# Optimization experiments

Measured on AMD Instinct MI355X. Metric: run time of the kernel, lower is better.

The kernel has to match this reference:

```python
import jax, jax.numpy as jnp
import numpy as np

LOG_0 = -1.0e30          # finite stand-in for log(0); avoids -inf NaNs under vjp
ACTIVE = -1.0e29         # anything above this is an 'active' beam
PRUNE_LOGIT = -9.0       # original skips extensions with log-prob <= -9


def _decode_one(probs, length, beam_width, blank_index):
    """CTC prefix beam search for one example. probs: [T, V] log-probs."""
    T, V = probs.shape
    Bw = beam_width
    t_idx = jnp.arange(T)
    v_idx = jnp.arange(V)
    b_idx = jnp.arange(Bw)

    def step(carry, inp):
        t, pr = inp  # pr: [V] log-probs at time t
        prefixes, lens, p_b, p_nb = carry
        p_tot = jnp.logaddexp(p_b, p_nb)
        act = p_tot > ACTIVE
        last = jnp.where(lens > 0, prefixes[b_idx, jnp.maximum(lens - 1, 0)], blank_index)
        # match[i, j]: prefix_i == prefix_j + [last_i]  (tree parent relation)
        eq = (prefixes[:, None, :] == prefixes[None, :, :]) | (t_idx[None, None, :] >= lens[None, :, None])
        match = eq.all(-1) & (lens[:, None] == lens[None, :] + 1) & act[None, :] & act[:, None]
        has_par = match.any(axis=1)
        par = jnp.argmax(match, axis=1)
        par_prev = jnp.where(has_par, jnp.where(last == last[par], p_b[par], p_tot[par]), LOG_0)
        # kept-beam (branch) update: label prob merges parent contribution, then emits last label
        cont_nb = jnp.where(lens > 0, jnp.logaddexp(p_nb, par_prev) + pr[last], LOG_0)
        cont_b = p_tot + pr[blank_index]
        # extension candidates [Bw, V]: p = probs[l] + (p_blank if l == last else p_total)
        prev_ext = jnp.where(v_idx[None, :] == last[:, None], p_b[:, None], p_tot[:, None])
        ext_nb = pr[None, :] + prev_ext
        # child already a live beam -> merged via branch update above, skip extension
        child_in = (jnp.zeros((Bw, V), jnp.int32).at[par, last].add(has_par.astype(jnp.int32)) > 0)
        bad = (v_idx[None, :] == blank_index) | (pr[None, :] <= PRUNE_LOGIT) | child_in | ~act[:, None]
        ext_nb = jnp.where(bad, LOG_0, ext_nb)
        # prune all candidates (Bw continuations + Bw*V extensions) to top beam_width
        all_pb = jnp.concatenate([cont_b, jnp.full((Bw * V,), LOG_0, cont_b.dtype)])
        all_pnb = jnp.concatenate([cont_nb, ext_nb.reshape(-1)])
        _, top = jax.lax.top_k(jnp.logaddexp(all_pb, all_pnb), Bw)
        is_ext = top >= Bw
        src = jnp.where(is_ext, (top - Bw) // V, top)
        lab = ((top - Bw) % V).astype(jnp.int32)  # garbage for continuations, masked below
        new_pref = prefixes[src]
        src_len = lens[src]
        put = is_ext[:, None] & (t_idx[None, :] == src_len[:, None])
        new_pref = jnp.where(put, lab[:, None], new_pref)
        new_lens = src_len + is_ext.astype(jnp.int32)
        new_pb = all_pb[top]
        new_pnb = all_pnb[top]
        live = t < length
        return (jnp.where(live, new_pref, prefixes),
                jnp.where(live, new_lens, lens),
                jnp.where(live, new_pb, p_b),
                jnp.where(live, new_pnb, p_nb)), None

    init = (jnp.full((Bw, T), -1, jnp.int32),
            jnp.zeros((Bw,), jnp.int32),
            jnp.full((Bw,), LOG_0, probs.dtype).at[0].set(0.0),  # root: blank prob = log(1)
            jnp.full((Bw,), LOG_0, probs.dtype))
    (prefixes, lens, p_b, p_nb), _ = jax.lax.scan(step, init, (t_idx, probs))
    totals = jnp.logaddexp(p_b, p_nb)
    best = jnp.argmax(totals)
    seq = jnp.where(t_idx < lens[best], prefixes[best], 0)
    return seq, lens[best], totals[best]


def setup_inputs() -> dict:
    key = jax.random.key(0)
    k1, k2 = jax.random.split(key)
    B, T, V = 128, 256, 128
    logits = jax.random.normal(k1, (B, T, V), jnp.float32) * 2.0
    probabilities = jax.nn.log_softmax(logits, axis=-1)  # module consumes log-probs
    lengths = jax.random.randint(k2, (B,), 1, T + 1, dtype=jnp.int32)
    return {"probabilities": probabilities, "lengths": lengths,
            "beam_width": 8, "blank_index": 0}


def reference(probabilities, lengths, beam_width, blank_index):
    dec = jax.vmap(lambda p, L: _decode_one(p, L, beam_width, blank_index))(probabilities, lengths)
    seqs, dec_lens, _scores = dec
    # decoded label sequences padded with 0 (to T), plus per-example decoded lengths
    return seqs, dec_lens
```

## Files before the change

kernel.cpp:

```cpp
#include <hip/hip_runtime.h>
#include <math.h>

#define LOG0f (-1.0e30f)
#define ACTIVE_TH (-1.0e29f)
#define PRUNE_TH (-9.0f)
#define VCAB 128
#define HSZ 4096
#define HMASK (HSZ - 1)
#define MAXN 2052
#define HEMPTY 0xFFFFFFFFu

__device__ __forceinline__ float lae(float a, float b) {
    float mx = fmaxf(a, b);
    float d = fabsf(a - b);
    return mx + log1pf(expf(-d));
}
__device__ __forceinline__ unsigned mono(float f) {
    unsigned u = __float_as_uint(f);
    return (u & 0x80000000u) ? ~u : (u | 0x80000000u);
}
__device__ __forceinline__ float mono_inv(unsigned m) {
    unsigned u = (m & 0x80000000u) ? (m & 0x7FFFFFFFu) : ~m;
    return __uint_as_float(u);
}
__device__ __forceinline__ unsigned rlaneu(unsigned x, int l) {
    return (unsigned)__builtin_amdgcn_readlane((int)x, l);
}
__device__ __forceinline__ float rlanef(float x, int l) {
    return __uint_as_float(rlaneu(__float_as_uint(x), l));
}
__device__ __forceinline__ unsigned sel8u(const unsigned a[8], unsigned s) {
    unsigned r = a[0];
#pragma unroll
    for (int j = 1; j < 8; ++j) r = (s == (unsigned)j) ? a[j] : r;
    return r;
}
__device__ __forceinline__ float sel8f(const float a[8], unsigned s) {
    float r = a[0];
#pragma unroll
    for (int j = 1; j < 8; ++j) r = (s == (unsigned)j) ? a[j] : r;
    return r;
}

__device__ __forceinline__ unsigned wred_max_u32(unsigned x) {
    unsigned y;
    y = (unsigned)__builtin_amdgcn_update_dpp(0, (int)x, 0x111, 0xf, 0xf, false);
    x = (y > x) ? y : x;
    y = (unsigned)__builtin_amdgcn_update_dpp(0, (int)x, 0x112, 0xf, 0xf, false);
    x = (y > x) ? y : x;
    y = (unsigned)__builtin_amdgcn_update_dpp(0, (int)x, 0x114, 0xf, 0xf, false);
    x = (y > x) ? y : x;
    y = (unsigned)__builtin_amdgcn_update_dpp(0, (int)x, 0x118, 0xf, 0xf, false);
    x = (y > x) ? y : x;
    y = (unsigned)__builtin_amdgcn_update_dpp(0, (int)x, 0x142, 0xa, 0xf, false);
    x = (y > x) ? y : x;
    y = (unsigned)__builtin_amdgcn_update_dpp(0, (int)x, 0x143, 0xc, 0xf, false);
    x = (y > x) ? y : x;
    return (unsigned)__builtin_amdgcn_readlane((int)x, 63);
}

__global__ __launch_bounds__(64)
void ctc_beam_kernel(const float* __restrict__ probs, const int* __restrict__ lengths,
                     const int* __restrict__ blank_p, int* __restrict__ out_seq,
                     int* __restrict__ out_len, int T) {
    __shared__ unsigned hsh[HSZ];
    __shared__ unsigned nodeinfo[MAXN];
    __shared__ int sh_seq[256];

    const int lane = threadIdx.x;
    const int b = blockIdx.x;
    const int blank = blank_p[0];
    const int length = lengths[b];
    const float* __restrict__ P = probs + (size_t)b * T * VCAB;
    const float4* __restrict__ P4 = (const float4*)P;
    const int own = lane & 7;
    const int slice = lane >> 3;
    const int vbase = slice * 16;

    for (int i = lane; i < HSZ; i += 64) hsh[i] = HEMPTY;
    __syncthreads();

    unsigned node8[8], par8[8], len8[8], last8[8];
#pragma unroll
    for (int j = 0; j < 8; ++j) {
        node8[j] = 0; par8[j] = 0xFFFu; len8[j] = 0; last8[j] = (unsigned)blank;
    }
    float pb_own = (own == 0) ? 0.0f : LOG0f;
    float pnb_own = LOG0f;
    int len_own = 0, last_own = blank;
    unsigned node_own = 0, par_own = 0xFFFu;

    float4 s0, s1, s2, s3;
    float prL, prH;
    {
        int base4 = (vbase >> 2);
        s0 = P4[base4]; s1 = P4[base4 + 1]; s2 = P4[base4 + 2]; s3 = P4[base4 + 3];
        prL = P[lane]; prH = P[64 + lane];
    }

#pragma clang loop unroll(disable)
    for (int t = 0; t < length; ++t) {
        float4 n0, n1, n2, n3;
        float nprL = 0.f, nprH = 0.f;
        n0 = n1 = n2 = n3 = make_float4(0.f, 0.f, 0.f, 0.f);
        if (t + 1 < length) {
            int base4 = (t + 1) * 32 + (vbase >> 2);
            n0 = P4[base4]; n1 = P4[base4 + 1]; n2 = P4[base4 + 2]; n3 = P4[base4 + 3];
            nprL = P[(size_t)(t + 1) * VCAB + lane];
            nprH = P[(size_t)(t + 1) * VCAB + 64 + lane];
        }

        float pt_own = lae(pb_own, pnb_own);
        unsigned long long bal = __ballot(pt_own > ACTIVE_TH);
        unsigned actmask = (unsigned)bal & 0xFFu;
        bool act_own = (actmask >> own) & 1u;

        float pb8[8], pt8[8];
#pragma unroll
        for (int j = 0; j < 8; ++j) {
            pb8[j] = rlanef(pb_own, j);
            pt8[j] = rlanef(pt_own, j);
        }
        float prB = (blank < 64) ? rlanef(prL, blank) : rlanef(prH, blank - 64);
        float prv8[8];
#pragma unroll
        for (int j = 0; j < 8; ++j) {
            int lj = (int)last8[j];
            float a = rlanef(prL, lj & 63), c2 = rlanef(prH, lj & 63);
            prv8[j] = (lj < 64) ? a : c2;
        }

        int p_own = 0;
        bool matched = false;
        {
            bool gate = act_own && (len_own > 0);
#pragma unroll
            for (int j = 0; j < 8; ++j) {
                bool m = gate && ((actmask >> j) & 1u) && (node8[j] == par_own);
                if (m) { p_own = j; matched = true; }
            }
        }
        float pbp = pb8[0], ptp = pt8[0];
        int lastp = (int)last8[0];
#pragma unroll
        for (int j = 1; j < 8; ++j) {
            bool m = (p_own == j);
            pbp = m ? pb8[j] : pbp;
            ptp = m ? pt8[j] : ptp;
            lastp = m ? (int)last8[j] : lastp;
        }
        float pprev = matched ? ((last_own == lastp) ? pbp : ptp) : LOG0f;
        float prLast = prv8[0];
#pragma unroll
        for (int j = 1; j < 8; ++j) prLast = (own == j) ? prv8[j] : prLast;

        float contb_own = pt_own + prB;
        float contnb_own = (len_own > 0) ? (lae(pnb_own, pprev) + prLast) : LOG0f;
        float tot_own = lae(contb_own, contnb_own);

        unsigned claimed16 = 0;
#pragma unroll
        for (int j = 0; j < 8; ++j) {
            bool mj = ((actmask >> j) & 1u) && act_own && (node_own == par8[j]);
            bool ins = ((last8[j] >> 4) == (unsigned)slice);
            claimed16 |= (mj && ins) ? (1u << (last8[j] & 15u)) : 0u;
        }

        unsigned long long K[17];
#define MAKEK(c, pv)                                                                     \
        {                                                                                \
            int v = vbase + (c);                                                         \
            float prev = (v == last_own) ? pb_own : pt_own;                              \
            float val = (pv) + prev;                                                     \
            bool bad = (v == blank) | ((pv) <= PRUNE_TH) | (!act_own) |                  \
                       (bool)((claimed16 >> (c)) & 1u);                                  \
            if (bad) val = LOG0f;                                                        \
            K[c] = (((unsigned long long)mono(val)) << 32) |                             \
                   (unsigned)~(8u + (unsigned)(own * VCAB + v));                         \
        }
        MAKEK(0, s0.x) MAKEK(1, s0.y) MAKEK(2, s0.z) MAKEK(3, s0.w)
        MAKEK(4, s1.x) MAKEK(5, s1.y) MAKEK(6, s1.z) MAKEK(7, s1.w)
        MAKEK(8, s2.x) MAKEK(9, s2.y) MAKEK(10, s2.z) MAKEK(11, s2.w)
        MAKEK(12, s3.x) MAKEK(13, s3.y) MAKEK(14, s3.z) MAKEK(15, s3.w)
#undef MAKEK
        K[16] = (lane < 8)
                    ? ((((unsigned long long)mono(tot_own)) << 32) | (unsigned)~(unsigned)lane)
                    : 0ull;

        unsigned long long m1 = 0ull, m2 = 0ull, m3 = 0ull;
#pragma unroll
        for (int k = 0; k < 17; ++k) {
            unsigned long long key = K[k];
            bool g1 = key > m1, g2 = key > m2, g3 = key > m3;
            unsigned long long t1 = g1 ? key : m1;
            unsigned long long t2 = g1 ? m1 : (g2 ? key : m2);
            m3 = (g1 | g2) ? m2 : (g3 ? key : m3);
            m1 = t1; m2 = t2;
        }

        unsigned long long W = ~0ull;
        unsigned selh[8], sell[8];
        bool dead = false;
#pragma unroll
        for (int r = 0; r < 8; ++r) {
            unsigned long long c = (m1 < W) ? m1 : ((m2 < W) ? m2 : ((m3 < W) ? m3 : 0ull));
            bool need = (c == 0ull) && !dead;
            if (__any(need)) {
                if (need) {
                    c = 0ull;
#pragma unroll
                    for (int k = 0; k < 17; ++k) {
                        bool g = (K[k] < W) && (K[k] > c);
                        c = g ? K[k] : c;
                    }
                    if (c == 0ull) dead = true;
                    else { m1 = c; m2 = ~0ull; m3 = ~0ull; }
                }
            }
            unsigned ch = (unsigned)(c >> 32), cl = (unsigned)c;
            unsigned M = wred_max_u32(ch);
            unsigned lo2 = (ch == M) ? cl : 0u;
            unsigned L = wred_max_u32(lo2);
            W = (((unsigned long long)M) << 32) | L;
            selh[r] = M; sell[r] = L;
        }

        float cb8[8], cn8[8];
#pragma unroll
        for (int j = 0; j < 8; ++j) {
            cb8[j] = rlanef(contb_own, j);
            cn8[j] = rlanef(contnb_own, j);
        }

        unsigned myM = sel8u(selh, (unsigned)own);
        unsigned myL = sel8u(sell, (unsigned)own);
        unsigned sel = ~myL;
        bool iscont = sel < 8u;
        unsigned e = sel - 8u;
        unsigned s = iscont ? sel : (e >> 7);
        unsigned lab = e & 127u;
        unsigned nd = sel8u(node8, s);
        unsigned pr = sel8u(par8, s);
        unsigned ln = sel8u(len8, s);
        unsigned la = sel8u(last8, s);
        float cbs = sel8f(cb8, s);
        float cns = sel8f(cn8, s);
        float npb_own = iscont ? cbs : LOG0f;
        float npnb_own = iscont ? cns : mono_inv(myM);
        unsigned A = iscont ? ((nd << 12) | pr) : nd;
        unsigned Bv = iscont ? ((ln << 7) | la) : (((ln + 1u) << 7) | lab);
        unsigned long long extbal = __ballot(!iscont);
        unsigned extmask = (unsigned)extbal & 0xFFu;

        unsigned insRes = 0;
        if ((extmask >> lane) & 1u) {
            unsigned preid = 1u + 8u * (unsigned)t + (unsigned)lane;
            unsigned hkey = (nd << 7) | lab;
            unsigned entry = (hkey << 12) | preid;
            unsigned h = ((hkey * 2654435761u) >> 20) & HMASK;
            for (;;) {
                unsigned prev = atomicCAS(&hsh[h], HEMPTY, entry);
                if (prev == HEMPTY) { nodeinfo[preid] = hkey; insRes = preid; break; }
                if ((prev >> 12) == hkey) { insRes = prev & 0xFFFu; break; }
                h = (h + 1) & HMASK;
            }
        }
#pragma unroll
        for (int r = 0; r < 8; ++r) {
            unsigned Ar = rlaneu(A, r);
            unsigned Br = rlaneu(Bv, r);
            unsigned nd2 = Ar >> 12;
            if ((extmask >> r) & 1u) nd2 = rlaneu(insRes, r);
            node8[r] = nd2; par8[r] = Ar & 0xFFFu;
            len8[r] = Br >> 7; last8[r] = Br & 127u;
        }
        node_own = sel8u(node8, (unsigned)own);
        par_own = sel8u(par8, (unsigned)own);
        len_own = (int)sel8u(len8, (unsigned)own);
        last_own = (int)sel8u(last8, (unsigned)own);
        pb_own = npb_own; pnb_own = npnb_own;

        s0 = n0; s1 = n1; s2 = n2; s3 = n3;
        prL = nprL; prH = nprH;
    }

    unsigned fh, fl;
    {
        float tot = lae(pb_own, pnb_own);
        fh = (lane < 8) ? mono(tot) : 0u;
        fl = (lane < 8) ? ~(unsigned)lane : 0u;
    }
    {
        unsigned M = wred_max_u32(fh);
        unsigned lo2 = (fh == M) ? fl : 0u;
        fl = wred_max_u32(lo2);
    }
    const int best = (int)(~fl);
    int L = 0;
    unsigned c = 0;
#pragma unroll
    for (int j = 0; j < 8; ++j)
        if (best == j) { L = (int)len8[j]; c = node8[j]; }
    if (lane == 0) {
        for (int k = L - 1; k >= 0; --k) {
            unsigned info = nodeinfo[c];
            sh_seq[k] = (int)(info & 127u);
            c = info >> 7;
        }
    }
    __syncthreads();
    for (int j = lane; j < T; j += 64)
        out_seq[(size_t)b * T + j] = (j < L) ? sh_seq[j] : 0;
    if (lane == 0) out_len[b] = L;
}

extern "C" void kernel_launch(void* const* d_in, const int* in_sizes, int n_in,
                              void* d_out, int out_size, void* d_ws, size_t ws_size,
                              hipStream_t stream) {
    const float* probs = (const float*)d_in[0];
    const int* lengths = (const int*)d_in[1];
    const int* blank_p = (const int*)d_in[3];
    const int B = in_sizes[1];
    const int T = in_sizes[0] / (B * VCAB);
    int* out = (int*)d_out;
    ctc_beam_kernel<<<B, 64, 0, stream>>>(probs, lengths, blank_p, out,
                                          out + (size_t)B * T, T);
}
```

Before: 1.286 ms.

## Split per-lane top-3 insertion into two chains and fast-path unique-max tie-break

Builds the per-lane top-3 from two independent insertion chains over the even and odd keys and merges them, which shortens the serial dependency chain. Each selection round skips the second wavefront max reduction when only one lane holds the max high word, and reads that lane's low word directly. The next-step prefetch becomes an unconditional clamped load, and the lookup arrays become macro-expanded scalars so they stay in registers. The changes add branching on ballot popcount and code size, and the two-list merge must reproduce the single-chain top-3 exactly.

```diff
diff --git a/kernel.cpp b/kernel.cpp
--- a/kernel.cpp
+++ b/kernel.cpp
@@ -35,12 +35,6 @@
     for (int j = 1; j < 8; ++j) r = (s == (unsigned)j) ? a[j] : r;
     return r;
 }
-__device__ __forceinline__ float sel8f(const float a[8], unsigned s) {
-    float r = a[0];
-#pragma unroll
-    for (int j = 1; j < 8; ++j) r = (s == (unsigned)j) ? a[j] : r;
-    return r;
-}
 
 __device__ __forceinline__ unsigned wred_max_u32(unsigned x) {
     unsigned y;
@@ -58,6 +52,17 @@
     x = (y > x) ? y : x;
     return (unsigned)__builtin_amdgcn_readlane((int)x, 63);
 }
+
+#define REP8(X) X(0) X(1) X(2) X(3) X(4) X(5) X(6) X(7)
+#define REP7(X) X(1) X(2) X(3) X(4) X(5) X(6) X(7)
+#define SEL8N(out, s, n)                                                        \
+    do {                                                                        \
+        out = n##_0;                                                            \
+        out = ((s) == 1u) ? n##_1 : out; out = ((s) == 2u) ? n##_2 : out;       \
+        out = ((s) == 3u) ? n##_3 : out; out = ((s) == 4u) ? n##_4 : out;       \
+        out = ((s) == 5u) ? n##_5 : out; out = ((s) == 6u) ? n##_6 : out;       \
+        out = ((s) == 7u) ? n##_7 : out;                                        \
+    } while (0)
 
 __global__ __launch_bounds__(64)
 void ctc_beam_kernel(const float* __restrict__ probs, const int* __restrict__ lengths,
@@ -100,14 +105,14 @@
 
 #pragma clang loop unroll(disable)
     for (int t = 0; t < length; ++t) {
+        const int tn = (t + 1 < length) ? (t + 1) : (length - 1);
         float4 n0, n1, n2, n3;
-        float nprL = 0.f, nprH = 0.f;
-        n0 = n1 = n2 = n3 = make_float4(0.f, 0.f, 0.f, 0.f);
-        if (t + 1 < length) {
-            int base4 = (t + 1) * 32 + (vbase >> 2);
+        float nprL, nprH;
+        {
+            int base4 = tn * 32 + (vbase >> 2);
             n0 = P4[base4]; n1 = P4[base4 + 1]; n2 = P4[base4 + 2]; n3 = P4[base4 + 3];
-            nprL = P[(size_t)(t + 1) * VCAB + lane];
-            nprH = P[(size_t)(t + 1) * VCAB + 64 + lane];
+            nprL = P[(size_t)tn * VCAB + lane];
+            nprH = P[(size_t)tn * VCAB + 64 + lane];
         }
 
         float pt_own = lae(pb_own, pnb_own);
@@ -115,44 +120,48 @@
         unsigned actmask = (unsigned)bal & 0xFFu;
         bool act_own = (actmask >> own) & 1u;
 
-        float pb8[8], pt8[8];
-#pragma unroll
-        for (int j = 0; j < 8; ++j) {
-            pb8[j] = rlanef(pb_own, j);
-            pt8[j] = rlanef(pt_own, j);
-        }
+#define TBL(j) float pb8_##j = rlanef(pb_own, j); float pt8_##j = rlanef(pt_own, j);
+        REP8(TBL)
+#undef TBL
         float prB = (blank < 64) ? rlanef(prL, blank) : rlanef(prH, blank - 64);
-        float prv8[8];
-#pragma unroll
-        for (int j = 0; j < 8; ++j) {
-            int lj = (int)last8[j];
-            float a = rlanef(prL, lj & 63), c2 = rlanef(prH, lj & 63);
-            prv8[j] = (lj < 64) ? a : c2;
-        }
+#define PRV(j)                                                                  \
+        float prv8_##j;                                                         \
+        {                                                                       \
+            int lj = (int)last8[j];                                             \
+            float a_ = rlanef(prL, lj & 63), c_ = rlanef(prH, lj & 63);         \
+            prv8_##j = (lj < 64) ? a_ : c_;                                     \
+        }
+        REP8(PRV)
+#undef PRV
 
         int p_own = 0;
         bool matched = false;
         {
             bool gate = act_own && (len_own > 0);
-#pragma unroll
-            for (int j = 0; j < 8; ++j) {
-                bool m = gate && ((actmask >> j) & 1u) && (node8[j] == par_own);
-                if (m) { p_own = j; matched = true; }
+#define PM(j)                                                                   \
+            {                                                                   \
+                bool m_ = gate && ((actmask >> j) & 1u) && (node8[j] == par_own); \
+                if (m_) { p_own = j; matched = true; }                          \
             }
-        }
-        float pbp = pb8[0], ptp = pt8[0];
+            REP8(PM)
+#undef PM
+        }
+        float pbp = pb8_0, ptp = pt8_0;
         int lastp = (int)last8[0];
-#pragma unroll
-        for (int j = 1; j < 8; ++j) {
-            bool m = (p_own == j);
-            pbp = m ? pb8[j] : pbp;
-            ptp = m ? pt8[j] : ptp;
-            lastp = m ? (int)last8[j] : lastp;
-        }
+#define PSEL(j)                                                                 \
+        {                                                                       \
+            bool m_ = (p_own == j);                                             \
+            pbp = m_ ? pb8_##j : pbp;                                           \
+            ptp = m_ ? pt8_##j : ptp;                                           \
+            lastp = m_ ? (int)last8[j] : lastp;                                 \
+        }
+        REP7(PSEL)
+#undef PSEL
         float pprev = matched ? ((last_own == lastp) ? pbp : ptp) : LOG0f;
-        float prLast = prv8[0];
-#pragma unroll
-        for (int j = 1; j < 8; ++j) prLast = (own == j) ? prv8[j] : prLast;
+        float prLast = prv8_0;
+#define PLSEL(j) prLast = (own == j) ? prv8_##j : prLast;
+        REP7(PLSEL)
+#undef PLSEL
 
         float contb_own = pt_own + prB;
         float contnb_own = (len_own > 0) ? (lae(pnb_own, pprev) + prLast) : LOG0f;
@@ -187,53 +196,80 @@
                     ? ((((unsigned long long)mono(tot_own)) << 32) | (unsigned)~(unsigned)lane)
                     : 0ull;
 
-        unsigned long long m1 = 0ull, m2 = 0ull, m3 = 0ull;
-#pragma unroll
-        for (int k = 0; k < 17; ++k) {
-            unsigned long long key = K[k];
-            bool g1 = key > m1, g2 = key > m2, g3 = key > m3;
-            unsigned long long t1 = g1 ? key : m1;
-            unsigned long long t2 = g1 ? m1 : (g2 ? key : m2);
-            m3 = (g1 | g2) ? m2 : (g3 ? key : m3);
-            m1 = t1; m2 = t2;
+        unsigned long long a1 = 0ull, a2 = 0ull, a3 = 0ull;
+        unsigned long long b1 = 0ull, b2 = 0ull, b3 = 0ull;
+#define INSC(t1v, t2v, t3v, key)                                                \
+        {                                                                       \
+            unsigned long long k_ = (key);                                      \
+            bool g1 = k_ > t1v, g2 = k_ > t2v, g3 = k_ > t3v;                   \
+            unsigned long long x1 = g1 ? k_ : t1v;                              \
+            unsigned long long x2 = g1 ? t1v : (g2 ? k_ : t2v);                 \
+            t3v = (g1 | g2) ? t2v : (g3 ? k_ : t3v);                            \
+            t1v = x1; t2v = x2;                                                 \
+        }
+        INSC(a1, a2, a3, K[0])  INSC(a1, a2, a3, K[2])  INSC(a1, a2, a3, K[4])
+        INSC(a1, a2, a3, K[6])  INSC(a1, a2, a3, K[8])  INSC(a1, a2, a3, K[10])
+        INSC(a1, a2, a3, K[12]) INSC(a1, a2, a3, K[14]) INSC(a1, a2, a3, K[16])
+        INSC(b1, b2, b3, K[1])  INSC(b1, b2, b3, K[3])  INSC(b1, b2, b3, K[5])
+        INSC(b1, b2, b3, K[7])  INSC(b1, b2, b3, K[9])  INSC(b1, b2, b3, K[11])
+        INSC(b1, b2, b3, K[13]) INSC(b1, b2, b3, K[15])
+#undef INSC
+        unsigned long long m1, m2, m3;
+        {
+            unsigned long long u = (a1 < b1) ? a1 : b1;
+            m1 = (a1 < b1) ? b1 : a1;
+            unsigned long long v = (a2 < b2) ? b2 : a2;
+            unsigned long long w = (a2 < b2) ? a2 : b2;
+            m2 = (u < v) ? v : u;
+            unsigned long long mn = (u < v) ? u : v;
+            unsigned long long X = (a2 > b1) ? a3 : ((b2 > a1) ? b3 : 0ull);
+            unsigned long long wX = (w < X) ? X : w;
+            m3 = (mn < wX) ? wX : mn;
         }
 
         unsigned long long W = ~0ull;
-        unsigned selh[8], sell[8];
+        unsigned selh_0, selh_1, selh_2, selh_3, selh_4, selh_5, selh_6, selh_7;
+        unsigned sell_0, sell_1, sell_2, sell_3, sell_4, sell_5, sell_6, sell_7;
         bool dead = false;
-#pragma unroll
-        for (int r = 0; r < 8; ++r) {
-            unsigned long long c = (m1 < W) ? m1 : ((m2 < W) ? m2 : ((m3 < W) ? m3 : 0ull));
-            bool need = (c == 0ull) && !dead;
-            if (__any(need)) {
-                if (need) {
-                    c = 0ull;
-#pragma unroll
-                    for (int k = 0; k < 17; ++k) {
-                        bool g = (K[k] < W) && (K[k] > c);
-                        c = g ? K[k] : c;
-                    }
-                    if (c == 0ull) dead = true;
-                    else { m1 = c; m2 = ~0ull; m3 = ~0ull; }
-                }
-            }
-            unsigned ch = (unsigned)(c >> 32), cl = (unsigned)c;
-            unsigned M = wred_max_u32(ch);
-            unsigned lo2 = (ch == M) ? cl : 0u;
-            unsigned L = wred_max_u32(lo2);
-            W = (((unsigned long long)M) << 32) | L;
-            selh[r] = M; sell[r] = L;
-        }
-
-        float cb8[8], cn8[8];
-#pragma unroll
-        for (int j = 0; j < 8; ++j) {
-            cb8[j] = rlanef(contb_own, j);
-            cn8[j] = rlanef(contnb_own, j);
-        }
-
-        unsigned myM = sel8u(selh, (unsigned)own);
-        unsigned myL = sel8u(sell, (unsigned)own);
+#define ROUND(r)                                                                         \
+        do {                                                                             \
+            unsigned long long c = (m1 < W) ? m1 : ((m2 < W) ? m2 : ((m3 < W) ? m3 : 0ull)); \
+            bool need = (c == 0ull) && !dead;                                            \
+            if (__any(need)) {                                                           \
+                if (need) {                                                              \
+                    c = 0ull;                                                            \
+                    _Pragma("unroll")                                                    \
+                    for (int k = 0; k < 17; ++k) {                                       \
+                        bool g = (K[k] < W) && (K[k] > c);                               \
+                        c = g ? K[k] : c;                                                \
+                    }                                                                    \
+                    if (c == 0ull) dead = true;                                          \
+                    else { m1 = c; m2 = ~0ull; m3 = ~0ull; }                             \
+                }                                                                        \
+            }                                                                            \
+            unsigned ch = (unsigned)(c >> 32), cl = (unsigned)c;                         \
+            unsigned M = wred_max_u32(ch);                                               \
+            unsigned long long tb = __ballot(ch == M);                                   \
+            unsigned L;                                                                  \
+            if (__builtin_popcountll(tb) == 1) {                                         \
+                L = rlaneu(cl, __builtin_ctzll(tb));                                     \
+            } else {                                                                     \
+                unsigned lo2 = (ch == M) ? cl : 0u;                                      \
+                L = wred_max_u32(lo2);                                                   \
+            }                                                                            \
+            W = (((unsigned long long)M) << 32) | L;                                     \
+            selh_##r = M; sell_##r = L;                                                  \
+        } while (0);
+        ROUND(0) ROUND(1) ROUND(2) ROUND(3) ROUND(4) ROUND(5) ROUND(6) ROUND(7)
+#undef ROUND
+
+#define CBT(j) float cb8_##j = rlanef(contb_own, j); float cn8_##j = rlanef(contnb_own, j);
+        REP8(CBT)
+#undef CBT
+
+        unsigned myM, myL;
+        SEL8N(myM, (unsigned)own, selh);
+        SEL8N(myL, (unsigned)own, sell);
         unsigned sel = ~myL;
         bool iscont = sel < 8u;
         unsigned e = sel - 8u;
@@ -243,8 +279,9 @@
         unsigned pr = sel8u(par8, s);
         unsigned ln = sel8u(len8, s);
         unsigned la = sel8u(last8, s);
-        float cbs = sel8f(cb8, s);
-        float cns = sel8f(cn8, s);
+        float cbs, cns;
+        SEL8N(cbs, s, cb8);
+        SEL8N(cns, s, cn8);
         float npb_own = iscont ? cbs : LOG0f;
         float npnb_own = iscont ? cns : mono_inv(myM);
         unsigned A = iscont ? ((nd << 12) | pr) : nd;
```

New measurement: 1.175 ms. 1.09x faster.
